# Kernel optimization log

Hardware: AMD Instinct MI355X
Metric: run time of the kernel (lower is better)

## Reference

```python
import jax, jax.numpy as jnp
from jax import lax
import numpy as np

B, N, D_MODEL = 4, 2048, 768
D_INNER = 1536      # int(2.0 * d_model)
DT_RANK = 48        # ceil(768 / 16)
EPS = 1e-5


def setup_inputs() -> dict:
    key = jax.random.key(0)
    ks = jax.random.split(key, 9)
    x = jax.random.normal(ks[0], (B, N, D_MODEL), jnp.float32)
    # BFS order: a permutation of node ids
    sorted_index = jax.random.permutation(ks[1], N).astype(jnp.int32)
    # parent BFS position of node at BFS position i, must be < i; root (i=0) has -1
    pos = jnp.arange(N)
    r = jax.random.randint(ks[2], (N,), 0, N)
    sorted_parent = jnp.where(pos == 0, -1, r % jnp.maximum(pos, 1)).astype(jnp.int32)
    s = 0.02
    in_proj_w = jax.random.normal(ks[3], (D_MODEL, 2 * D_INNER), jnp.float32) * s
    x_proj_w = jax.random.normal(ks[4], (D_INNER, DT_RANK + 2), jnp.float32) * s
    dt_proj_w = jax.random.normal(ks[5], (DT_RANK, D_INNER), jnp.float32) * (DT_RANK ** -0.5)
    # dt bias init: softplus^{-1}(dt) with dt ~ LogUniform(1e-3, 1e-1)
    dt = jnp.exp(jax.random.uniform(ks[6], (D_INNER,)) * (np.log(0.1) - np.log(0.001)) + np.log(0.001))
    dt_proj_b = (dt + jnp.log(-jnp.expm1(-dt))).astype(jnp.float32)
    A_log = jnp.zeros((D_INNER,), jnp.float32)   # log(A=1) per original init (d_state=1)
    D_param = jnp.ones((D_INNER,), jnp.float32)
    ln_gamma = jnp.ones((D_INNER,), jnp.float32)
    ln_beta = jnp.zeros((D_INNER,), jnp.float32)
    out_proj_w = jax.random.normal(ks[7], (D_INNER, D_MODEL), jnp.float32) * s
    return dict(x=x, sorted_index=sorted_index, sorted_parent=sorted_parent,
                in_proj_w=in_proj_w, x_proj_w=x_proj_w, dt_proj_w=dt_proj_w,
                dt_proj_b=dt_proj_b, A_log=A_log, D_param=D_param,
                ln_gamma=ln_gamma, ln_beta=ln_beta, out_proj_w=out_proj_w)


def _tree_ssm_recurrence(dBx, dA, sorted_index, sorted_parent):
    """h[bfs i] = dA[node(i)] * h[parent_bfs(i)] + dBx[node(i)]. Inputs (B,N,Di) node-major."""
    b, n, di = dBx.shape
    dA_bfs = jnp.take(dA, sorted_index, axis=1)    # (B,N,Di) in BFS order
    dBx_bfs = jnp.take(dBx, sorted_index, axis=1)

    def step(h_buf, inp):
        t, par, dA_t, dBx_t = inp                   # dA_t/dBx_t: (B,Di)
        h_par = h_buf[:, jnp.maximum(par, 0)]       # (B,Di) gather at parent BFS pos
        h_par = jnp.where(par < 0, jnp.zeros_like(h_par), h_par)
        h_t = dA_t * h_par + dBx_t
        return h_buf.at[:, t].set(h_t), h_t

    xs = (jnp.arange(n), sorted_parent,
          dA_bfs.transpose(1, 0, 2), dBx_bfs.transpose(1, 0, 2))
    _, h_bfs = lax.scan(step, jnp.zeros((b, n, di), dBx.dtype), xs)
    # scatter BFS-order states back to node-id order
    h = jnp.zeros((b, n, di), dBx.dtype).at[:, sorted_index].set(h_bfs.transpose(1, 0, 2))
    return h


def reference(x, sorted_index, sorted_parent, in_proj_w, x_proj_w, dt_proj_w,
              dt_proj_b, A_log, D_param, ln_gamma, ln_beta, out_proj_w):
    xz = x @ in_proj_w                              # (B,N,2*Di)
    x_inner, z = jnp.split(xz, 2, axis=-1)
    z = jax.nn.silu(z)
    x_dbl = x_inner @ x_proj_w                      # (B,N,dt_rank+2)
    dt_lr, B_ssm, C_ssm = (x_dbl[..., :DT_RANK], x_dbl[..., DT_RANK:DT_RANK + 1],
                           x_dbl[..., DT_RANK + 1:DT_RANK + 2])
    dt = jax.nn.softplus(dt_lr @ dt_proj_w + dt_proj_b)  # (B,N,Di)
    As = -jnp.exp(A_log)                            # (Di,) negative
    dA = jnp.exp(dt * As)                           # (B,N,Di) in (0,1)
    dBx = dt * B_ssm * x_inner                      # (B,N,Di)
    h = _tree_ssm_recurrence(dBx, dA, sorted_index, sorted_parent)
    y = h * C_ssm + D_param * x_inner               # (B,N,Di)
    mu = jnp.mean(y, axis=-1, keepdims=True)
    var = jnp.mean(jnp.square(y - mu), axis=-1, keepdims=True)
    y = (y - mu) * lax.rsqrt(var + EPS) * ln_gamma + ln_beta
    y = y * z
    return y @ out_proj_w                           # (B,N,D)
```

## Files before the change

kernel.cpp:

```cpp
#include <hip/hip_runtime.h>
#include <math.h>


#define ROWS 8192
#define DIN 1536
#define DMOD 768
#define NSEQ 2048
#define DTR 48
#define NSPLIT 4

typedef __bf16 bfrag __attribute__((ext_vector_type(8)));
typedef float f4 __attribute__((ext_vector_type(4)));

__device__ __forceinline__ unsigned short f2bf(float f) {
  unsigned int u = __float_as_uint(f);
  unsigned int r = (u + 0x7fffu + ((u >> 16) & 1u)) >> 16;
  return (unsigned short)r;
}
__device__ __forceinline__ float bf2f(unsigned short h) {
  return __uint_as_float(((unsigned int)h) << 16);
}

__device__ __forceinline__ void gld_lds16(const void* g, void* l) {
  __builtin_amdgcn_global_load_lds((const __attribute__((address_space(1))) void*)g,
                                   (__attribute__((address_space(3))) void*)l, 16, 0, 0);
}

__device__ __forceinline__ void barx() {
  asm volatile("" ::: "memory");
  __builtin_amdgcn_s_barrier();
  asm volatile("" ::: "memory");
}

__global__ __launch_bounds__(512, 1) void gemm256_silu(
    const unsigned short* __restrict__ A, const unsigned short* __restrict__ Bt,
    unsigned short* __restrict__ XI, unsigned short* __restrict__ Z, int K) {
  __shared__ unsigned short lds[2][(256 + 192) * 64];
  const int tid = threadIdx.x;
  const int w = tid >> 6, l = tid & 63;
  const int quad = l >> 4, l16 = l & 15;
  const int wr = w >> 2, wc = w & 3;
  const int row0 = blockIdx.y * 256, col0 = blockIdx.x * 192;
  const int nt = K >> 6;

  const int srow = tid >> 3;
  const int schunk = ((tid & 7) ^ (srow & 7)) * 8;
  const unsigned short* aS = A + (size_t)(row0 + srow) * K + schunk;
  const unsigned short* bS = Bt + (size_t)(col0 + srow) * K + schunk;

#define STG_A(bufi, q, kt)                                     \
  gld_lds16(aS + (size_t)((q) * 64) * K + (size_t)(kt) * 64,   \
            (char*)&lds[bufi][(q) * 4096] + w * 1024)
#define STG_B(bufi, q, kt)                                     \
  gld_lds16(bS + (size_t)((q) * 64) * K + (size_t)(kt) * 64,   \
            (char*)&lds[bufi][16384 + (q) * 4096] + w * 1024)

  const int arow = (wr * 128 + l16) * 64;
  const int brow = (wc * 48 + l16) * 64;
  int cs[2];
  cs[0] = (quad ^ (l16 & 7)) * 8;
  cs[1] = ((4 + quad) ^ (l16 & 7)) * 8;

#define RDA(m, ks) (*(const bfrag*)(const void*)(LA + arow + (m) * 1024 + cs[ks]))
#define RDB(n, ks) (*(const bfrag*)(const void*)(LB + brow + (n) * 1024 + cs[ks]))

  f4 acc[8][3];
#pragma unroll
  for (int m = 0; m < 8; m++)
#pragma unroll
    for (int n = 0; n < 3; n++) acc[m][n] = (f4){0.f, 0.f, 0.f, 0.f};

  const int kt1 = (nt > 1) ? 1 : 0;
#pragma unroll
  for (int q = 0; q < 4; q++) STG_A(0, q, 0);
#pragma unroll
  for (int q = 0; q < 3; q++) STG_B(0, q, 0);
#pragma unroll
  for (int q = 0; q < 4; q++) STG_A(1, q, kt1);
#pragma unroll
  for (int q = 0; q < 3; q++) STG_B(1, q, kt1);
  asm volatile("s_waitcnt vmcnt(7)" ::: "memory");
  barx();

  for (int t = 0; t < nt; ++t) {
    const int b = t & 1;
    const unsigned short* LA = &lds[b][0];
    const unsigned short* LB = &lds[b][16384];
    const int kA = (t + 2 < nt) ? (t + 2) : (nt - 1);
    bfrag af[4][2], bfr[3][2];

#pragma unroll
    for (int m = 0; m < 4; m++) {
      af[m][0] = RDA(m, 0);
      af[m][1] = RDA(m, 1);
    }
#pragma unroll
    for (int n = 0; n < 2; n++) {
      bfr[n][0] = RDB(n, 0);
      bfr[n][1] = RDB(n, 1);
    }
    barx();
    __builtin_amdgcn_s_setprio(1);
#pragma unroll
    for (int m = 0; m < 4; m++)
#pragma unroll
      for (int n = 0; n < 2; n++) {
        acc[m][n] = __builtin_amdgcn_mfma_f32_16x16x32_bf16(af[m][0], bfr[n][0], acc[m][n], 0, 0, 0);
        acc[m][n] = __builtin_amdgcn_mfma_f32_16x16x32_bf16(af[m][1], bfr[n][1], acc[m][n], 0, 0, 0);
      }
    __builtin_amdgcn_s_setprio(0);
    barx();

    bfr[2][0] = RDB(2, 0);
    bfr[2][1] = RDB(2, 1);
    barx();
    __builtin_amdgcn_s_setprio(1);
#pragma unroll
    for (int m = 0; m < 4; m++) {
      acc[m][2] = __builtin_amdgcn_mfma_f32_16x16x32_bf16(af[m][0], bfr[2][0], acc[m][2], 0, 0, 0);
      acc[m][2] = __builtin_amdgcn_mfma_f32_16x16x32_bf16(af[m][1], bfr[2][1], acc[m][2], 0, 0, 0);
    }
    __builtin_amdgcn_s_setprio(0);
    barx();

    STG_A(b, 0, kA);
    STG_A(b, 2, kA);
    STG_B(b, 0, kA);
    STG_B(b, 1, kA);
#pragma unroll
    for (int m = 0; m < 4; m++) {
      af[m][0] = RDA(m + 4, 0);
      af[m][1] = RDA(m + 4, 1);
    }
    barx();
    __builtin_amdgcn_s_setprio(1);
#pragma unroll
    for (int m = 0; m < 4; m++)
#pragma unroll
      for (int n = 0; n < 2; n++) {
        acc[m + 4][n] = __builtin_amdgcn_mfma_f32_16x16x32_bf16(af[m][0], bfr[n][0], acc[m + 4][n], 0, 0, 0);
        acc[m + 4][n] = __builtin_amdgcn_mfma_f32_16x16x32_bf16(af[m][1], bfr[n][1], acc[m + 4][n], 0, 0, 0);
      }
    __builtin_amdgcn_s_setprio(0);
    barx();

    STG_A(b, 1, kA);
    STG_A(b, 3, kA);
    STG_B(b, 2, kA);
    barx();
    __builtin_amdgcn_s_setprio(1);
#pragma unroll
    for (int m = 0; m < 4; m++) {
      acc[m + 4][2] = __builtin_amdgcn_mfma_f32_16x16x32_bf16(af[m][0], bfr[2][0], acc[m + 4][2], 0, 0, 0);
      acc[m + 4][2] = __builtin_amdgcn_mfma_f32_16x16x32_bf16(af[m][1], bfr[2][1], acc[m + 4][2], 0, 0, 0);
    }
    __builtin_amdgcn_s_setprio(0);
    asm volatile("s_waitcnt vmcnt(7)" ::: "memory");
    barx();
  }
  asm volatile("s_waitcnt vmcnt(0)" ::: "memory");

#undef STG_A
#undef STG_B
#undef RDA
#undef RDB

  const bool is_z = (col0 >= DIN);
  unsigned short* dst = is_z ? Z : XI;
  const int cb = col0 + wc * 48 + l16 - (is_z ? DIN : 0);
#pragma unroll
  for (int m = 0; m < 8; m++) {
    const int rb = row0 + wr * 128 + m * 16 + quad * 4;
#pragma unroll
    for (int n = 0; n < 3; n++)
#pragma unroll
      for (int r = 0; r < 4; r++) {
        float v = acc[m][n][r];
        if (is_z) v = v / (1.f + __expf(-v));
        dst[(size_t)(rb + r) * DIN + cb + n * 16] = f2bf(v);
      }
  }
}

template <int MODE>
__global__ __launch_bounds__(256) void mfma_gemm(
    const unsigned short* __restrict__ A, const unsigned short* __restrict__ Bt,
    void* __restrict__ C0v, void* __restrict__ C1v, int K, int ldc) {
  __shared__ unsigned short As[128 * 32];
  __shared__ unsigned short Bs[128 * 32];
  const int tid = threadIdx.x;
  const int w = tid >> 6, l = tid & 63;
  const int quad = l >> 4, l16 = l & 15;
  const int wrow = (w >> 1) * 64, wcol = (w & 1) * 64;
  const int row0 = blockIdx.y * 128, col0 = blockIdx.x * 128;

  f4 acc[4][4];
#pragma unroll
  for (int i = 0; i < 4; i++)
#pragma unroll
    for (int j = 0; j < 4; j++) acc[i][j] = (f4){0.f, 0.f, 0.f, 0.f};

  const int arow = row0 + w * 16 + (l >> 2);
  const int brow = col0 + w * 16 + (l >> 2);
  const int kcol = (((l & 3) ^ ((l >> 2) & 3)) * 8);
  const int qs = (quad ^ (l16 & 3)) * 8;

  for (int k0 = 0; k0 < K; k0 += 32) {
#pragma unroll
    for (int r = 0; r < 2; r++) {
      gld_lds16(A + (size_t)(arow + r * 64) * K + k0 + kcol,
                (char*)As + r * 4096 + w * 1024);
      gld_lds16(Bt + (size_t)(brow + r * 64) * K + k0 + kcol,
                (char*)Bs + r * 4096 + w * 1024);
    }
    __syncthreads();
    bfrag af[4], bf[4];
#pragma unroll
    for (int i = 0; i < 4; i++)
      af[i] = *(const bfrag*)(const void*)(As + (wrow + i * 16 + l16) * 32 + qs);
#pragma unroll
    for (int j = 0; j < 4; j++)
      bf[j] = *(const bfrag*)(const void*)(Bs + (wcol + j * 16 + l16) * 32 + qs);
#pragma unroll
    for (int i = 0; i < 4; i++)
#pragma unroll
      for (int j = 0; j < 4; j++)
        acc[i][j] = __builtin_amdgcn_mfma_f32_16x16x32_bf16(af[i], bf[j], acc[i][j], 0, 0, 0);
    __syncthreads();
  }

  if (MODE == 0) {
    float* C0 = (float*)C0v;
    const int ccol = col0 + wcol + l16;
#pragma unroll
    for (int i = 0; i < 4; i++) {
      const int rb = row0 + wrow + i * 16 + quad * 4;
#pragma unroll
      for (int j = 0; j < 4; j++)
#pragma unroll
        for (int r = 0; r < 4; r++)
          C0[(size_t)(rb + r) * ldc + ccol + j * 16] = acc[i][j][r];
    }
  } else {
    const bool is_z = (col0 >= DIN);
    unsigned short* dst = is_z ? (unsigned short*)C1v : (unsigned short*)C0v;
    const int cbase = col0 + wcol + l16 - (is_z ? DIN : 0);
#pragma unroll
    for (int i = 0; i < 4; i++) {
      const int rb = row0 + wrow + i * 16 + quad * 4;
#pragma unroll
      for (int j = 0; j < 4; j++)
#pragma unroll
        for (int r = 0; r < 4; r++) {
          float v = acc[i][j][r];
          if (is_z) v = v / (1.f + __expf(-v));
          dst[(size_t)(rb + r) * DIN + cbase + j * 16] = f2bf(v);
        }
    }
  }
}

__global__ __launch_bounds__(1024) void prep1_kernel(
    const int* __restrict__ sidx, const int* __restrict__ spar,
    int* __restrict__ SLOT_PACK, int* __restrict__ SLOTINV,
    int* __restrict__ LSTART, int* __restrict__ NLEV,
    const float* __restrict__ x, unsigned short* __restrict__ Xbf,
    const float* __restrict__ xpw, unsigned short* __restrict__ XPW,
    const float* __restrict__ dtw, unsigned short* __restrict__ DTWb,
    const float* __restrict__ A_log, float* __restrict__ negA) {
  const int bi = blockIdx.x;
  const int tid = threadIdx.x;
  if (bi == 0) {
    __shared__ int par[2048], idx[2048], ancA[2048], ancB[2048], rnkA[2048], rnkB[2048];
    __shared__ int dmax;
    for (int i = tid; i < 2048; i += 1024) {
      const int p = spar[i];
      par[i] = p;
      idx[i] = sidx[i];
      ancA[i] = (p < 0) ? -1 : p;
      rnkA[i] = (p < 0) ? 0 : 1;
    }
    if (tid == 0) dmax = 0;
    __syncthreads();
    for (int r = 0; r < 11; r++) {
      int* ca = (r & 1) ? ancB : ancA;
      int* cr = (r & 1) ? rnkB : rnkA;
      int* na = (r & 1) ? ancA : ancB;
      int* nr = (r & 1) ? rnkA : rnkB;
      for (int i = tid; i < 2048; i += 1024) {
        const int a = ca[i], rv = cr[i];
        if (a >= 0) {
          nr[i] = rv + cr[a];
          na[i] = ca[a];
        } else {
          nr[i] = rv;
          na[i] = a;
        }
      }
      __syncthreads();
    }
    for (int i = tid; i < 2048; i += 1024) ancA[i] = 0;
    __syncthreads();
    for (int i = tid; i < 2048; i += 1024) {
      atomicAdd(&ancA[rnkB[i]], 1);
      atomicMax(&dmax, rnkB[i]);
    }
    __syncthreads();
    for (int s = 0; s < 11; s++) {
      const int off = 1 << s;
      int* cur = (s & 1) ? ancB : ancA;
      int* nxt = (s & 1) ? ancA : ancB;
      for (int i = tid; i < 2048; i += 1024) {
        int v = cur[i];
        if (i >= off) v += cur[i - off];
        nxt[i] = v;
      }
      __syncthreads();
    }
    for (int i = tid; i < 2049; i += 1024) {
      const int v = (i == 0) ? 0 : ancB[i - 1];
      LSTART[i] = v;
      if (i < 2048) rnkA[i] = v;
    }
    if (tid == 0) NLEV[0] = dmax + 1;
    __syncthreads();
    for (int i = tid; i < 2048; i += 1024) {
      const int d = rnkB[i];
      const int slot = atomicAdd(&rnkA[d], 1);
      const int node = idx[i];
      const int p = par[i];
      const int pn = (p < 0) ? -1 : idx[p];
      SLOT_PACK[slot] = node | ((pn + 1) << 12);
      SLOTINV[node] = slot;
    }
  } else if (bi < 1 + 1536) {
    const int i = ((bi - 1) * 1024 + tid) * 4;
    const float4 v = *(const float4*)(x + i);
    union { unsigned short h[4]; uint2 u; } pk;
    pk.h[0] = f2bf(v.x);
    pk.h[1] = f2bf(v.y);
    pk.h[2] = f2bf(v.z);
    pk.h[3] = f2bf(v.w);
    *(uint2*)(Xbf + i) = pk.u;
  } else if (bi < 1 + 1536 + 96) {
    const int i = (bi - 1537) * 1024 + tid;
    const int c = i / 1536, k = i % 1536;
    XPW[i] = (c < 50) ? f2bf(xpw[(size_t)k * 50 + c]) : (unsigned short)0;
  } else if (bi < 1 + 1536 + 96 + 96) {
    const int i = (bi - 1633) * 1024 + tid;
    const int d = i >> 6, k = i & 63;
    DTWb[i] = (k < 48) ? f2bf(dtw[(size_t)k * DIN + d]) : (unsigned short)0;
  } else {
    const int i = (bi - 1729) * 1024 + tid;
    if (i < DIN) negA[i] = -__expf(A_log[i]);
  }
}

__global__ __launch_bounds__(256) void prep2_kernel(
    const float* __restrict__ W1, unsigned short* __restrict__ W1t,
    const float* __restrict__ W2, unsigned short* __restrict__ W2t) {
  __shared__ float t[32][33];
  int idx = blockIdx.x;
  const float* W;
  unsigned short* Wt;
  int K, N, n0, k0;
  if (idx < 2304) {
    W = W1; Wt = W1t; K = DMOD; N = 2 * DIN;
    n0 = (idx % 96) * 32; k0 = (idx / 96) * 32;
  } else {
    idx -= 2304;
    W = W2; Wt = W2t; K = DIN; N = DMOD;
    n0 = (idx % 24) * 32; k0 = (idx / 24) * 32;
  }
  const int tx = threadIdx.x & 31, ty = threadIdx.x >> 5;
  for (int i = ty; i < 32; i += 8) t[i][tx] = W[(size_t)(k0 + i) * N + n0 + tx];
  __syncthreads();
  for (int i = ty; i < 32; i += 8)
    Wt[(size_t)(n0 + i) * K + k0 + tx] = f2bf(t[tx][i]);
}

__global__ __launch_bounds__(256) void xdbl_mfma(
    const unsigned short* __restrict__ XI, const unsigned short* __restrict__ XPW,
    float* __restrict__ XP) {
  __shared__ unsigned short As[128 * 32];
  __shared__ unsigned short Bs[64 * 32];
  const int tid = threadIdx.x;
  const int w = tid >> 6, l = tid & 63;
  const int quad = l >> 4, l16 = l & 15;
  const int split = blockIdx.x;
  const int row0 = blockIdx.y * 128;
  const int kbase = split * (DIN / NSPLIT);

  f4 acc[2][4];
#pragma unroll
  for (int i = 0; i < 2; i++)
#pragma unroll
    for (int j = 0; j < 4; j++) acc[i][j] = (f4){0.f, 0.f, 0.f, 0.f};

  const int srow = w * 16 + (l >> 2);
  const int kcol = (((l & 3) ^ ((l >> 2) & 3)) * 8);
  const int qs = (quad ^ (l16 & 3)) * 8;

  for (int c = 0; c < 12; c++) {
    const int k0 = kbase + c * 32;
#pragma unroll
    for (int r = 0; r < 2; r++) {
      gld_lds16(XI + (size_t)(row0 + srow + r * 64) * DIN + k0 + kcol,
                (char*)As + r * 4096 + w * 1024);
    }
    gld_lds16(XPW + (size_t)srow * DIN + k0 + kcol, (char*)Bs + w * 1024);
    __syncthreads();
    bfrag af[2], bf[4];
#pragma unroll
    for (int i = 0; i < 2; i++)
      af[i] = *(const bfrag*)(const void*)(As + (w * 32 + i * 16 + l16) * 32 + qs);
#pragma unroll
    for (int j = 0; j < 4; j++)
      bf[j] = *(const bfrag*)(const void*)(Bs + (j * 16 + l16) * 32 + qs);
#pragma unroll
    for (int i = 0; i < 2; i++)
#pragma unroll
      for (int j = 0; j < 4; j++)
        acc[i][j] = __builtin_amdgcn_mfma_f32_16x16x32_bf16(af[i], bf[j], acc[i][j], 0, 0, 0);
    __syncthreads();
  }

  float* dst = XP + (size_t)split * ROWS * 64 + (size_t)row0 * 64;
#pragma unroll
  for (int i = 0; i < 2; i++) {
    const int rb = w * 32 + i * 16 + quad * 4;
#pragma unroll
    for (int j = 0; j < 4; j++) {
      const int col = j * 16 + l16;
#pragma unroll
      for (int r = 0; r < 4; r++) dst[(size_t)(rb + r) * 64 + col] = acc[i][j][r];
    }
  }
}

__global__ __launch_bounds__(256) void xp_reduce(
    const float* __restrict__ XP, unsigned short* __restrict__ DTLRb,
    float* __restrict__ BCv, float* __restrict__ CCv) {
  const int i = blockIdx.x * 256 + threadIdx.x;
  const int row = i >> 4, c4 = (i & 15) * 4;
  const float* p = XP + (size_t)row * 64 + c4;
  float4 s = make_float4(0.f, 0.f, 0.f, 0.f);
#pragma unroll
  for (int sp = 0; sp < NSPLIT; sp++) {
    const float4 v = *(const float4*)(p + (size_t)sp * ROWS * 64);
    s.x += v.x;
    s.y += v.y;
    s.z += v.z;
    s.w += v.w;
  }
  if (c4 == 48) {
    BCv[row] = s.x;
    CCv[row] = s.y;
  }
  union { unsigned short h[4]; uint2 u; } pk;
  pk.h[0] = f2bf(s.x);
  pk.h[1] = f2bf(s.y);
  pk.h[2] = f2bf(s.z);
  pk.h[3] = f2bf(s.w);
  *(uint2*)(DTLRb + (size_t)row * 64 + c4) = pk.u;
}

__global__ __launch_bounds__(256) void dt_gemm(
    const unsigned short* __restrict__ DTLRb, const unsigned short* __restrict__ DTWb,
    const float* __restrict__ bias, const float* __restrict__ negA,
    const float* __restrict__ BCv, const unsigned short* __restrict__ XI,
    const int* __restrict__ SLOTINV,
    unsigned short* __restrict__ DAp, unsigned short* __restrict__ DBXp) {
  __shared__ unsigned short As[2][64 * 32];
  __shared__ unsigned short Bs[2][128 * 32];
  __shared__ int sinv[64];
  __shared__ float bcs[64];
  const int tid = threadIdx.x;
  const int w = tid >> 6, l = tid & 63;
  const int quad = l >> 4, l16 = l & 15;
  const int wrow = (w >> 1) * 32, wcol = (w & 1) * 64;
  const int row0 = blockIdx.y * 64, col0 = blockIdx.x * 128;
  const int p0 = row0 & (NSEQ - 1);
  const int bbase = row0 & ~(NSEQ - 1);
  const int srow = w * 16 + (l >> 2);
  const int koff = (((l & 3) ^ ((l >> 2) & 3)) * 8);
  const int qs = (quad ^ (l16 & 3)) * 8;

#pragma unroll
  for (int c = 0; c < 2; c++) {
    gld_lds16(DTLRb + (size_t)(row0 + srow) * 64 + c * 32 + koff,
              (char*)As[c] + w * 1024);
#pragma unroll
    for (int r = 0; r < 2; r++)
      gld_lds16(DTWb + (size_t)(col0 + srow + r * 64) * 64 + c * 32 + koff,
                (char*)Bs[c] + r * 4096 + w * 1024);
  }
  if (tid < 64) {
    sinv[tid] = SLOTINV[p0 + tid];
    bcs[tid] = BCv[row0 + tid];
  }
  __syncthreads();

  f4 acc[2][4];
#pragma unroll
  for (int i = 0; i < 2; i++)
#pragma unroll
    for (int j = 0; j < 4; j++) acc[i][j] = (f4){0.f, 0.f, 0.f, 0.f};

#pragma unroll
  for (int c = 0; c < 2; c++) {
    bfrag af[2], bf[4];
#pragma unroll
    for (int i = 0; i < 2; i++)
      af[i] = *(const bfrag*)(const void*)(As[c] + (wrow + i * 16 + l16) * 32 + qs);
#pragma unroll
    for (int j = 0; j < 4; j++)
      bf[j] = *(const bfrag*)(const void*)(Bs[c] + (wcol + j * 16 + l16) * 32 + qs);
#pragma unroll
    for (int i = 0; i < 2; i++)
#pragma unroll
      for (int j = 0; j < 4; j++)
        acc[i][j] = __builtin_amdgcn_mfma_f32_16x16x32_bf16(af[i], bf[j], acc[i][j], 0, 0, 0);
  }

  float bj[4], aj[4];
#pragma unroll
  for (int j = 0; j < 4; j++) {
    const int d = col0 + wcol + j * 16 + l16;
    bj[j] = bias[d];
    aj[j] = negA[d];
  }
#pragma unroll
  for (int i = 0; i < 2; i++) {
#pragma unroll
    for (int r = 0; r < 4; r++) {
      const int row_l = wrow + i * 16 + quad * 4 + r;
      const int row = row0 + row_l;
      const float bc = bcs[row_l];
      const size_t rp = (size_t)(bbase + sinv[row_l]) * DIN;
#pragma unroll
      for (int j = 0; j < 4; j++) {
        const int d = col0 + wcol + j * 16 + l16;
        const float s = acc[i][j][r] + bj[j];
        const float sp = fmaxf(s, 0.f) + __logf(1.f + __expf(-fabsf(s)));
        const float xi = bf2f(XI[(size_t)row * DIN + d]);
        DAp[rp + d] = f2bf(__expf(sp * aj[j]));
        DBXp[rp + d] = f2bf(sp * bc * xi);
      }
    }
  }
}

__global__ __launch_bounds__(256) void recur_kernel(
    const unsigned short* __restrict__ DAp, const unsigned short* __restrict__ DBXp,
    unsigned short* __restrict__ Hb,
    const int* __restrict__ SLOT_PACK, const int* __restrict__ LSTART,
    const int* __restrict__ NLEV) {
  __shared__ unsigned short hl[NSEQ * 16];
  __shared__ int spack[NSEQ];
  __shared__ int lst[258];
  const int tid = threadIdx.x;
  const int c8a = blockIdx.x * 2;
  const int b = c8a / 192;
  const int d8a = c8a % 192;
  const int nlev = NLEV[0];
  for (int i = tid; i < NSEQ; i += 256) spack[i] = SLOT_PACK[i];
  const int nl = (nlev + 1 < 258) ? nlev + 1 : 258;
  for (int i = tid; i < nl; i += 256) lst[i] = LSTART[i];
  __syncthreads();

  for (int L = 0; L < nlev; L++) {
    const int s0 = (L < 257) ? lst[L] : LSTART[L];
    const int s1 = (L + 1 < 258) ? lst[L + 1] : LSTART[L + 1];
    const int items = (s1 - s0) * 2;
    for (int it = tid; it < items; it += 256) {
      const int s = s0 + (it >> 1);
      const int ch = it & 1;
      const size_t goff = (size_t)(b * NSEQ + s) * DIN + (d8a + ch) * 8;
      union { uint4 u; unsigned short h[8]; } da, dbx, hpu, hvu;
      da.u = *(const uint4*)(DAp + goff);
      dbx.u = *(const uint4*)(DBXp + goff);
      const int pk = spack[s];
      const int node = pk & 4095;
      const int pn = (pk >> 12) - 1;
      float hp[8];
      if (pn >= 0) {
        hpu.u = *(const uint4*)(hl + pn * 16 + ch * 8);
#pragma unroll
        for (int e = 0; e < 8; e++) hp[e] = bf2f(hpu.h[e]);
      } else {
#pragma unroll
        for (int e = 0; e < 8; e++) hp[e] = 0.f;
      }
#pragma unroll
      for (int e = 0; e < 8; e++) {
        const float hv = fmaf(bf2f(da.h[e]), hp[e], bf2f(dbx.h[e]));
        hvu.h[e] = f2bf(hv);
      }
      *(uint4*)(hl + node * 16 + ch * 8) = hvu.u;
    }
    __syncthreads();
  }

  for (int i = tid; i < NSEQ * 2; i += 256) {
    const int node = i >> 1, ch = i & 1;
    *(uint4*)(Hb + (size_t)(b * NSEQ + node) * DIN + (d8a + ch) * 8) =
        *(const uint4*)(hl + node * 16 + ch * 8);
  }
}

__global__ __launch_bounds__(256) void ln_kernel(
    const unsigned short* __restrict__ Hb, const float* __restrict__ CCv,
    const unsigned short* __restrict__ XI, const float* __restrict__ Dp,
    const float* __restrict__ gamma, const float* __restrict__ beta,
    const unsigned short* __restrict__ Z, unsigned short* __restrict__ YLN) {
  const int row = blockIdx.x;
  const int tid = threadIdx.x;
  const float C = CCv[row];
  const unsigned short* hrow = Hb + (size_t)row * DIN;
  const unsigned short* xrow = XI + (size_t)row * DIN;
  float y[6];
  float s = 0.f, s2 = 0.f;
#pragma unroll
  for (int i = 0; i < 6; i++) {
    const int d = tid + i * 256;
    const float v = fmaf(bf2f(hrow[d]), C, Dp[d] * bf2f(xrow[d]));
    y[i] = v;
    s += v;
    s2 = fmaf(v, v, s2);
  }
#pragma unroll
  for (int off = 32; off >= 1; off >>= 1) {
    s += __shfl_down(s, off);
    s2 += __shfl_down(s2, off);
  }
  __shared__ float rs[4], rs2[4];
  const int w = tid >> 6;
  if ((tid & 63) == 0) {
    rs[w] = s;
    rs2[w] = s2;
  }
  __syncthreads();
  const float ts = rs[0] + rs[1] + rs[2] + rs[3];
  const float ts2 = rs2[0] + rs2[1] + rs2[2] + rs2[3];
  const float mu = ts * (1.f / 1536.f);
  const float var = ts2 * (1.f / 1536.f) - mu * mu;
  const float inv = rsqrtf(var + 1e-5f);
  unsigned short* yrow = YLN + (size_t)row * DIN;
  const unsigned short* zrow = Z + (size_t)row * DIN;
#pragma unroll
  for (int i = 0; i < 6; i++) {
    const int d = tid + i * 256;
    const float o = (y[i] - mu) * inv * gamma[d] + beta[d];
    yrow[d] = f2bf(o * bf2f(zrow[d]));
  }
}

extern "C" void kernel_launch(void* const* d_in, const int* in_sizes, int n_in,
                              void* d_out, int out_size, void* d_ws, size_t ws_size,
                              hipStream_t stream) {
  const float* x = (const float*)d_in[0];
  const int* sidx = (const int*)d_in[1];
  const int* spar = (const int*)d_in[2];
  const float* in_proj = (const float*)d_in[3];
  const float* x_proj = (const float*)d_in[4];
  const float* dt_proj = (const float*)d_in[5];
  const float* dt_b = (const float*)d_in[6];
  const float* A_log = (const float*)d_in[7];
  const float* Dp = (const float*)d_in[8];
  const float* gamma = (const float*)d_in[9];
  const float* beta = (const float*)d_in[10];
  const float* out_proj = (const float*)d_in[11];
  float* out = (float*)d_out;

  char* p = (char*)d_ws;
  const size_t RC = (size_t)ROWS * DIN;
  unsigned short* XI = (unsigned short*)p;   p += RC * 2;
  unsigned short* Z = (unsigned short*)p;    p += RC * 2;
  unsigned short* DAp = (unsigned short*)p;  p += RC * 2;
  unsigned short* DBXp = (unsigned short*)p; p += RC * 2;
  unsigned short* Hb = (unsigned short*)p;   p += RC * 2;
  float* XP = (float*)p;                     p += (size_t)NSPLIT * ROWS * 64 * 4;
  unsigned short* DTLRb = (unsigned short*)p; p += (size_t)ROWS * 64 * 2;
  float* BCv = (float*)p;                    p += ROWS * 4;
  float* CCv = (float*)p;                    p += ROWS * 4;
  float* negA = (float*)p;                   p += DIN * 4;
  unsigned short* Xbf = (unsigned short*)p;  p += (size_t)ROWS * DMOD * 2;
  unsigned short* W1t = (unsigned short*)p;  p += (size_t)2 * DIN * DMOD * 2;
  unsigned short* W2t = (unsigned short*)p;  p += (size_t)DMOD * DIN * 2;
  unsigned short* XPW = (unsigned short*)p;  p += (size_t)64 * DIN * 2;
  unsigned short* DTWb = (unsigned short*)p; p += (size_t)DIN * 64 * 2;
  int* ipart = (int*)p;
  int* SLOT_PACK = ipart;
  int* SLOTINV = ipart + 2048;
  int* LSTART = ipart + 4096;
  int* NLEV = ipart + 4096 + 2049;
  unsigned short* YLN = DAp;

  prep1_kernel<<<1731, 1024, 0, stream>>>(sidx, spar, SLOT_PACK, SLOTINV,
                                          LSTART, NLEV, x, Xbf, x_proj, XPW,
                                          dt_proj, DTWb, A_log, negA);
  prep2_kernel<<<3456, 256, 0, stream>>>(in_proj, W1t, out_proj, W2t);
  gemm256_silu<<<dim3(16, 32), 512, 0, stream>>>(Xbf, W1t, XI, Z, DMOD);
  xdbl_mfma<<<dim3(NSPLIT, 64), 256, 0, stream>>>(XI, XPW, XP);
  xp_reduce<<<ROWS * 16 / 256, 256, 0, stream>>>(XP, DTLRb, BCv, CCv);
  dt_gemm<<<dim3(12, 128), 256, 0, stream>>>(DTLRb, DTWb, dt_b, negA, BCv, XI,
                                             SLOTINV, DAp, DBXp);
  recur_kernel<<<384, 256, 0, stream>>>(DAp, DBXp, Hb, SLOT_PACK, LSTART, NLEV);
  ln_kernel<<<ROWS, 256, 0, stream>>>(Hb, CCv, XI, Dp, gamma, beta, Z, YLN);
  mfma_gemm<0><<<dim3(6, 64), 256, 0, stream>>>(YLN, W2t, out, nullptr, DIN, DMOD);
}
```

Measured before the change: 317.3 us.

## Swizzle block order for XCD locality and stage GEMM epilogue through LDS

Remaps the linear block id so that consecutive blocks dispatched round-robin across the 8 XCDs cover contiguous tiles, improving L2 reuse of A/B panels in the in-proj, generic, and x_proj GEMMs. The in-proj epilogue now writes bf16 results into LDS first, then stores 16-byte vectors row-contiguously to global memory instead of scattered 2-byte stores. This adds an extra barrier pair and LDS round trip, and the swizzle assumes a fixed grid shape of 16x32 for the in-proj kernel and 4x64 for the x_proj kernel.

```diff
diff --git a/kernel.cpp b/kernel.cpp
--- a/kernel.cpp
+++ b/kernel.cpp
@@ -40,7 +40,9 @@
   const int w = tid >> 6, l = tid & 63;
   const int quad = l >> 4, l16 = l & 15;
   const int wr = w >> 2, wc = w & 3;
-  const int row0 = blockIdx.y * 256, col0 = blockIdx.x * 192;
+  const int h = blockIdx.x + 16 * blockIdx.y;
+  const int swz = (h & 7) * 64 + (h >> 3);
+  const int row0 = (swz >> 4) * 256, col0 = (swz & 15) * 192;
   const int nt = K >> 6;
 
   const int srow = tid >> 3;
@@ -166,19 +168,31 @@
 #undef RDB
 
   const bool is_z = (col0 >= DIN);
-  unsigned short* dst = is_z ? Z : XI;
-  const int cb = col0 + wc * 48 + l16 - (is_z ? DIN : 0);
+  unsigned short* cl = (unsigned short*)&lds[0][0];
+  barx();
 #pragma unroll
   for (int m = 0; m < 8; m++) {
-    const int rb = row0 + wr * 128 + m * 16 + quad * 4;
-#pragma unroll
-    for (int n = 0; n < 3; n++)
+    const int rb = wr * 128 + m * 16 + quad * 4;
+#pragma unroll
+    for (int n = 0; n < 3; n++) {
+      const int cc = wc * 48 + n * 16 + l16;
 #pragma unroll
       for (int r = 0; r < 4; r++) {
         float v = acc[m][n][r];
         if (is_z) v = v / (1.f + __expf(-v));
-        dst[(size_t)(rb + r) * DIN + cb + n * 16] = f2bf(v);
+        cl[(rb + r) * 200 + cc] = f2bf(v);
       }
+    }
+  }
+  barx();
+  unsigned short* dstbase =
+      (is_z ? Z : XI) + (size_t)row0 * DIN + (col0 - (is_z ? DIN : 0));
+#pragma unroll
+  for (int i = 0; i < 12; i++) {
+    const int c = tid + i * 512;
+    const int row = c / 24, off = (c % 24) * 8;
+    *(uint4*)(dstbase + (size_t)row * DIN + off) =
+        *(const uint4*)(cl + row * 200 + off);
   }
 }
 
@@ -192,7 +206,11 @@
   const int w = tid >> 6, l = tid & 63;
   const int quad = l >> 4, l16 = l & 15;
   const int wrow = (w >> 1) * 64, wcol = (w & 1) * 64;
-  const int row0 = blockIdx.y * 128, col0 = blockIdx.x * 128;
+  const int h = blockIdx.x + gridDim.x * blockIdx.y;
+  const int nb = gridDim.x * gridDim.y;
+  int swz = h;
+  if ((nb & 7) == 0) swz = (h & 7) * (nb >> 3) + (h >> 3);
+  const int row0 = (swz / gridDim.x) * 128, col0 = (swz % gridDim.x) * 128;
 
   f4 acc[4][4];
 #pragma unroll
@@ -387,8 +405,10 @@
   const int tid = threadIdx.x;
   const int w = tid >> 6, l = tid & 63;
   const int quad = l >> 4, l16 = l & 15;
-  const int split = blockIdx.x;
-  const int row0 = blockIdx.y * 128;
+  const int h = blockIdx.x + 4 * blockIdx.y;
+  const int swz = (h & 7) * 32 + (h >> 3);
+  const int split = swz & 3;
+  const int row0 = (swz >> 2) * 128;
   const int kbase = split * (DIN / NSPLIT);
 
   f4 acc[2][4];
```

After: 310.0 us. 2.3% less time.

## Add XCD-aware block swizzle to GEMMs and merge gemm256 phases into two stages

Applied to the files above, without the earlier changes.

Remaps block indices in four GEMM kernels so consecutive blocks on the same XCD (blockIdx mod 8) cover contiguous tiles, aiming to improve L2 locality across MI355X's chiplets. It also restructures the main in_proj GEMM loop from four MFMA phases per k-tile to two. All three B fragments are now read up front and the global-to-LDS staging is regrouped around fewer barriers. This cuts barrier and sync overhead but raises register pressure and changes how loads overlap compute. The swizzle formulas are hardcoded to grid sizes, which is a risk if those sizes change.

```diff
diff --git a/kernel.cpp b/kernel.cpp
--- a/kernel.cpp
+++ b/kernel.cpp
@@ -40,7 +40,9 @@
   const int w = tid >> 6, l = tid & 63;
   const int quad = l >> 4, l16 = l & 15;
   const int wr = w >> 2, wc = w & 3;
-  const int row0 = blockIdx.y * 256, col0 = blockIdx.x * 192;
+  const int h = blockIdx.x + 16 * blockIdx.y;
+  const int swz = (h & 7) * 64 + (h >> 3);
+  const int row0 = (swz >> 4) * 256, col0 = (swz & 15) * 192;
   const int nt = K >> 6;
 
   const int srow = tid >> 3;
@@ -95,7 +97,7 @@
       af[m][1] = RDA(m, 1);
     }
 #pragma unroll
-    for (int n = 0; n < 2; n++) {
+    for (int n = 0; n < 3; n++) {
       bfr[n][0] = RDB(n, 0);
       bfr[n][1] = RDB(n, 1);
     }
@@ -104,56 +106,34 @@
 #pragma unroll
     for (int m = 0; m < 4; m++)
 #pragma unroll
-      for (int n = 0; n < 2; n++) {
+      for (int n = 0; n < 3; n++) {
         acc[m][n] = __builtin_amdgcn_mfma_f32_16x16x32_bf16(af[m][0], bfr[n][0], acc[m][n], 0, 0, 0);
         acc[m][n] = __builtin_amdgcn_mfma_f32_16x16x32_bf16(af[m][1], bfr[n][1], acc[m][n], 0, 0, 0);
       }
     __builtin_amdgcn_s_setprio(0);
     barx();
 
-    bfr[2][0] = RDB(2, 0);
-    bfr[2][1] = RDB(2, 1);
-    barx();
-    __builtin_amdgcn_s_setprio(1);
 #pragma unroll
     for (int m = 0; m < 4; m++) {
-      acc[m][2] = __builtin_amdgcn_mfma_f32_16x16x32_bf16(af[m][0], bfr[2][0], acc[m][2], 0, 0, 0);
-      acc[m][2] = __builtin_amdgcn_mfma_f32_16x16x32_bf16(af[m][1], bfr[2][1], acc[m][2], 0, 0, 0);
-    }
-    __builtin_amdgcn_s_setprio(0);
-    barx();
-
+      af[m][0] = RDA(m + 4, 0);
+      af[m][1] = RDA(m + 4, 1);
+    }
     STG_A(b, 0, kA);
     STG_A(b, 2, kA);
     STG_B(b, 0, kA);
     STG_B(b, 1, kA);
-#pragma unroll
-    for (int m = 0; m < 4; m++) {
-      af[m][0] = RDA(m + 4, 0);
-      af[m][1] = RDA(m + 4, 1);
-    }
+    STG_B(b, 2, kA);
     barx();
+    STG_A(b, 1, kA);
+    STG_A(b, 3, kA);
     __builtin_amdgcn_s_setprio(1);
 #pragma unroll
     for (int m = 0; m < 4; m++)
 #pragma unroll
-      for (int n = 0; n < 2; n++) {
+      for (int n = 0; n < 3; n++) {
         acc[m + 4][n] = __builtin_amdgcn_mfma_f32_16x16x32_bf16(af[m][0], bfr[n][0], acc[m + 4][n], 0, 0, 0);
         acc[m + 4][n] = __builtin_amdgcn_mfma_f32_16x16x32_bf16(af[m][1], bfr[n][1], acc[m + 4][n], 0, 0, 0);
       }
-    __builtin_amdgcn_s_setprio(0);
-    barx();
-
-    STG_A(b, 1, kA);
-    STG_A(b, 3, kA);
-    STG_B(b, 2, kA);
-    barx();
-    __builtin_amdgcn_s_setprio(1);
-#pragma unroll
-    for (int m = 0; m < 4; m++) {
-      acc[m + 4][2] = __builtin_amdgcn_mfma_f32_16x16x32_bf16(af[m][0], bfr[2][0], acc[m + 4][2], 0, 0, 0);
-      acc[m + 4][2] = __builtin_amdgcn_mfma_f32_16x16x32_bf16(af[m][1], bfr[2][1], acc[m + 4][2], 0, 0, 0);
-    }
     __builtin_amdgcn_s_setprio(0);
     asm volatile("s_waitcnt vmcnt(7)" ::: "memory");
     barx();
@@ -192,7 +172,11 @@
   const int w = tid >> 6, l = tid & 63;
   const int quad = l >> 4, l16 = l & 15;
   const int wrow = (w >> 1) * 64, wcol = (w & 1) * 64;
-  const int row0 = blockIdx.y * 128, col0 = blockIdx.x * 128;
+  const int h = blockIdx.x + gridDim.x * blockIdx.y;
+  const int nb = gridDim.x * gridDim.y;
+  int swz = h;
+  if ((nb & 7) == 0) swz = (h & 7) * (nb >> 3) + (h >> 3);
+  const int row0 = (swz / gridDim.x) * 128, col0 = (swz % gridDim.x) * 128;
 
   f4 acc[4][4];
 #pragma unroll
@@ -387,8 +371,10 @@
   const int tid = threadIdx.x;
   const int w = tid >> 6, l = tid & 63;
   const int quad = l >> 4, l16 = l & 15;
-  const int split = blockIdx.x;
-  const int row0 = blockIdx.y * 128;
+  const int h = blockIdx.x + 4 * blockIdx.y;
+  const int swz = (h & 7) * 32 + (h >> 3);
+  const int split = swz & 3;
+  const int row0 = (swz >> 2) * 128;
   const int kbase = split * (DIN / NSPLIT);
 
   f4 acc[2][4];
@@ -479,7 +465,9 @@
   const int w = tid >> 6, l = tid & 63;
   const int quad = l >> 4, l16 = l & 15;
   const int wrow = (w >> 1) * 32, wcol = (w & 1) * 64;
-  const int row0 = blockIdx.y * 64, col0 = blockIdx.x * 128;
+  const int h = blockIdx.x + 12 * blockIdx.y;
+  const int swz = (h & 7) * 192 + (h >> 3);
+  const int row0 = (swz / 12) * 64, col0 = (swz % 12) * 128;
   const int p0 = row0 & (NSEQ - 1);
   const int bbase = row0 & ~(NSEQ - 1);
   const int srow = w * 16 + (l >> 2);
```

Result: faster. 305.3 us (-3.8%).
